# Kernel tuning notes

Measured on AMD Instinct MI355X. Metric: run time of the kernel, lower is better.

The kernel has to match this reference:

```python
import jax, jax.numpy as jnp
import numpy as np

D_IN, D_HID = 64, 128

def _ff(x, w1, b1, w2, b2):
    # FeedForward: Linear -> ReLU -> Linear
    return jax.nn.relu(x @ w1 + b1) @ w2 + b2

def setup_inputs() -> dict:
    key = jax.random.key(0)
    ks = jax.random.split(key, 10)
    N, m = 8, 2048
    def lin(k, fan_in, fan_out):
        bound = 1.0 / np.sqrt(fan_in)
        return jax.random.uniform(k, (fan_in, fan_out), jnp.float32, -bound, bound)
    return {
        "x": jax.random.normal(ks[0], (N, m, D_IN), jnp.float32),
        "edge": jax.random.uniform(ks[1], (N, m, m), jnp.float32),
        # f: dim_in -> dim_hid//2 -> dim_hid
        "f_w1": lin(ks[2], D_IN, D_HID // 2),
        "f_b1": jnp.zeros((D_HID // 2,), jnp.float32),
        "f_w2": lin(ks[3], D_HID // 2, D_HID),
        "f_b2": jnp.zeros((D_HID,), jnp.float32),
        # g: 2*dim_in -> dim_hid -> dim_hid
        "g_w1": lin(ks[4], 2 * D_IN, D_HID),
        "g_b1": jnp.zeros((D_HID,), jnp.float32),
        "g_w2": lin(ks[5], D_HID, D_HID),
        "g_b2": jnp.zeros((D_HID,), jnp.float32),
    }

def reference(x, edge, f_w1, f_b1, f_w2, f_b2, g_w1, g_b1, g_w2, g_b2):
    # self dynamics: f(x) -> [N, m, D_HID]
    self_dyn = _ff(x, f_w1, f_b1, f_w2, f_b2)
    # Original builds interaction[n,i,j] = cat(x[n,i], x[n,i]) (receiver is
    # transposed twice), so g is constant along j. Compute g once per sender node.
    gx = _ff(jnp.concatenate([x, x], axis=-1), g_w1, g_b1, g_w2, g_b2)  # [N, m, H]
    # interaction.sum over sender dim i with edge weights: out[n,j] = sum_i edge[n,i,j]*gx[n,i]
    inter = jnp.einsum('nij,nih->njh', edge, gx)
    return self_dyn + inter
```

## Files before the change

### kernel.cpp

```cpp
#include <hip/hip_runtime.h>


typedef __attribute__((ext_vector_type(8))) short bf16x8;
typedef __attribute__((ext_vector_type(8))) unsigned short u16x8;
typedef __attribute__((ext_vector_type(4))) unsigned short u16x4;
typedef __attribute__((ext_vector_type(4))) float f32x4;
typedef __attribute__((ext_vector_type(8))) float f32x8;

static __device__ __forceinline__ unsigned short f2bf(float f) {
  union { float f; unsigned int i; } c; c.f = f;
  return (unsigned short)((c.i + 0x7fffu + ((c.i >> 16) & 1u)) >> 16);
}

__global__ __launch_bounds__(256) void k_gx(
    const float* __restrict__ x,
    const float* __restrict__ gw1,
    const float* __restrict__ gb1,
    const float* __restrict__ gw2,
    const float* __restrict__ gb2,
    unsigned short* __restrict__ gxT)
{
  __shared__ short xs[64 * 64];
  __shared__ short w1T[128 * 64];
  __shared__ short w2T[128 * 128];
  __shared__ short h2s[64 * 128];

  const int t = threadIdx.x;
  const int R0 = blockIdx.x * 64;

  for (int idx = t; idx < 64 * 128; idx += 256) {
    int k = idx >> 7, n = idx & 127;
    float v = gw1[idx] + gw1[64 * 128 + idx];
    w1T[(n << 6) + (((k >> 3) ^ (n & 7)) << 3) + (k & 7)] = (short)f2bf(v);
  }
  for (int idx = t; idx < 128 * 128; idx += 256) {
    int k = idx >> 7, n = idx & 127;
    w2T[(n << 7) + (((k >> 3) ^ (n & 7)) << 3) + (k & 7)] = (short)f2bf(gw2[idx]);
  }
  for (int s = t; s < 64 * 16; s += 256) {
    int row = s >> 4, c4 = s & 15;
    f32x4 v = *(const f32x4*)(x + (size_t)(R0 + row) * 64 + c4 * 4);
    u16x4 pk;
#pragma unroll
    for (int r = 0; r < 4; ++r) pk[r] = f2bf(v[r]);
    *(u16x4*)(xs + (row << 6) + (((c4 >> 1) ^ (row & 7)) << 3) + ((c4 & 1) << 2)) = pk;
  }
  __syncthreads();

  const int w = t >> 6, l = t & 63;
  const int lr = l & 15, q = l >> 4;
  const int mrow = w * 16 + lr;

  bf16x8 a[2];
#pragma unroll
  for (int ks = 0; ks < 2; ++ks) {
    int c = ks * 4 + q;
    a[ks] = *(const bf16x8*)(xs + (mrow << 6) + ((c ^ (mrow & 7)) << 3));
  }

  f32x4 acc;
#pragma unroll
  for (int nf = 0; nf < 8; ++nf) {
    acc = (f32x4){0.f, 0.f, 0.f, 0.f};
#pragma unroll
    for (int ks = 0; ks < 2; ++ks) {
      int c = ks * 4 + q;
      int nr = nf * 16 + lr;
      bf16x8 b = *(const bf16x8*)(w1T + (nr << 6) + ((c ^ (nr & 7)) << 3));
      acc = __builtin_amdgcn_mfma_f32_16x16x32_bf16(a[ks], b, acc, 0, 0, 0);
    }
    float bias = gb1[nf * 16 + lr];
#pragma unroll
    for (int r = 0; r < 4; ++r) {
      float v = acc[r] + bias;
      v = v > 0.f ? v : 0.f;
      int row = w * 16 + q * 4 + r, n = nf * 16 + lr;
      h2s[(row << 7) + (((n >> 3) ^ (row & 7)) << 3) + (n & 7)] = (short)f2bf(v);
    }
  }
  __syncthreads();

  bf16x8 a2[4];
#pragma unroll
  for (int ks = 0; ks < 4; ++ks) {
    int c = ks * 4 + q;
    a2[ks] = *(const bf16x8*)(h2s + (mrow << 7) + ((c ^ (mrow & 7)) << 3));
  }
  const int batch = R0 >> 11;
  const int ib = R0 & 2047;
#pragma unroll
  for (int nf = 0; nf < 8; ++nf) {
    acc = (f32x4){0.f, 0.f, 0.f, 0.f};
#pragma unroll
    for (int ks = 0; ks < 4; ++ks) {
      int c = ks * 4 + q;
      int nr = nf * 16 + lr;
      bf16x8 b = *(const bf16x8*)(w2T + (nr << 7) + ((c ^ (nr & 7)) << 3));
      acc = __builtin_amdgcn_mfma_f32_16x16x32_bf16(a2[ks], b, acc, 0, 0, 0);
    }
    float bias = gb2[nf * 16 + lr];
    u16x4 pk;
#pragma unroll
    for (int r = 0; r < 4; ++r) pk[r] = f2bf(acc[r] + bias);
    *(u16x4*)(gxT + (size_t)(batch * 128 + nf * 16 + lr) * 2048 + ib + w * 16 + q * 4) = pk;
  }
}

__device__ __forceinline__ void load_tiles(const float* ep, const unsigned short* gp,
                                           f32x8& er, u16x8 gr[4])
{
  er = *(const f32x8*)ep;
#pragma unroll
  for (int qq = 0; qq < 4; ++qq)
    gr[qq] = *(const u16x8*)(gp + (size_t)qq * 32 * 2048);
}

__global__ __launch_bounds__(256) void k_main(
    const float* __restrict__ edge,
    const unsigned short* __restrict__ gxT,
    const float* __restrict__ x,
    const float* __restrict__ fw1,
    const float* __restrict__ fb1,
    const float* __restrict__ fw2,
    const float* __restrict__ fb2,
    float* __restrict__ out)
{
  __shared__ short eT[32 * 72];
  __shared__ short bT[128 * 64];
  __shared__ short xs[32 * 64];
  __shared__ short w1T[64 * 64];
  __shared__ short h1s[32 * 64];

  const int t = threadIdx.x;
  const int batch = blockIdx.x & 7;
  const int j0 = (blockIdx.x >> 3) * 32;

  const int w = t >> 6, l = t & 63;
  const int wm = w & 1, wn = w >> 1;
  const int lr = l & 15, q = l >> 4;

  const int e_ii = t >> 2;
  const int e_cj = t & 3;
  const int g_hh = t >> 3;
  const int g_ci = t & 7;

  const float* ep = edge + (size_t)batch * 2048 * 2048 + (size_t)e_ii * 2048 + j0 + e_cj * 8;
  const unsigned short* gp = gxT + (size_t)batch * 128 * 2048 + (size_t)g_hh * 2048 + g_ci * 8;

  f32x4 acc[4];
#pragma unroll
  for (int nf = 0; nf < 4; ++nf) acc[nf] = (f32x4){0.f, 0.f, 0.f, 0.f};

  f32x8 er;
  u16x8 gr[4];
  load_tiles(ep, gp, er, gr);

  for (int kk = 0; kk < 32; ++kk) {
    __syncthreads();
#pragma unroll
    for (int u = 0; u < 8; ++u)
      eT[(e_cj * 8 + u) * 72 + (((e_ii >> 3) ^ e_cj) << 3) + (e_ii & 7)] = (short)f2bf(er[u]);
#pragma unroll
    for (int qq = 0; qq < 4; ++qq) {
      int r = qq * 32 + g_hh;
      *(u16x8*)(bT + (r << 6) + ((g_ci ^ (r & 7)) << 3)) = gr[qq];
    }
    __syncthreads();
    if (kk < 31) {
      ep += 64 * 2048; gp += 64;
      load_tiles(ep, gp, er, gr);
    }

#pragma unroll
    for (int ks = 0; ks < 2; ++ks) {
      const int c = ks * 4 + q;
      const int jj = wm * 16 + lr;
      bf16x8 a = *(const bf16x8*)(eT + jj * 72 + ((c ^ (jj >> 3)) << 3));
      bf16x8 b[4];
#pragma unroll
      for (int nf = 0; nf < 4; ++nf) {
        int h = wn * 64 + nf * 16 + lr;
        b[nf] = *(const bf16x8*)(bT + (h << 6) + ((c ^ (h & 7)) << 3));
      }
#pragma unroll
      for (int nf = 0; nf < 4; ++nf)
        acc[nf] = __builtin_amdgcn_mfma_f32_16x16x32_bf16(a, b[nf], acc[nf], 0, 0, 0);
    }
  }

  __syncthreads();
  for (int idx = t; idx < 64 * 64; idx += 256) {
    int k = idx >> 6, n = idx & 63;
    w1T[(n << 6) + (((k >> 3) ^ (n & 7)) << 3) + (k & 7)] = (short)f2bf(fw1[idx]);
  }
  for (int idx = t; idx < 64 * 128; idx += 256) {
    int k = idx >> 7, n = idx & 127;
    bT[(n << 6) + (((k >> 3) ^ (n & 7)) << 3) + (k & 7)] = (short)f2bf(fw2[idx]);
  }
  for (int s = t; s < 32 * 16; s += 256) {
    int row = s >> 4, c4 = s & 15;
    f32x4 v = *(const f32x4*)(x + (size_t)(batch * 2048 + j0 + row) * 64 + c4 * 4);
    u16x4 pk;
#pragma unroll
    for (int r = 0; r < 4; ++r) pk[r] = f2bf(v[r]);
    *(u16x4*)(xs + (row << 6) + (((c4 >> 1) ^ (row & 7)) << 3) + ((c4 & 1) << 2)) = pk;
  }
  __syncthreads();

  const int mrow = wm * 16 + lr;
  if (wn == 0) {
    bf16x8 a1[2];
#pragma unroll
    for (int ks = 0; ks < 2; ++ks) {
      int c = ks * 4 + q;
      a1[ks] = *(const bf16x8*)(xs + (mrow << 6) + ((c ^ (mrow & 7)) << 3));
    }
#pragma unroll
    for (int nf = 0; nf < 4; ++nf) {
      f32x4 h = (f32x4){0.f, 0.f, 0.f, 0.f};
#pragma unroll
      for (int ks = 0; ks < 2; ++ks) {
        int c = ks * 4 + q;
        int nr = nf * 16 + lr;
        bf16x8 b = *(const bf16x8*)(w1T + (nr << 6) + ((c ^ (nr & 7)) << 3));
        h = __builtin_amdgcn_mfma_f32_16x16x32_bf16(a1[ks], b, h, 0, 0, 0);
      }
      float bias = fb1[nf * 16 + lr];
#pragma unroll
      for (int r = 0; r < 4; ++r) {
        float v = h[r] + bias;
        v = v > 0.f ? v : 0.f;
        int row = wm * 16 + q * 4 + r, n = nf * 16 + lr;
        h1s[(row << 6) + (((n >> 3) ^ (row & 7)) << 3) + (n & 7)] = (short)f2bf(v);
      }
    }
  }
  __syncthreads();

  bf16x8 a2[2];
#pragma unroll
  for (int ks = 0; ks < 2; ++ks) {
    int c = ks * 4 + q;
    a2[ks] = *(const bf16x8*)(h1s + (mrow << 6) + ((c ^ (mrow & 7)) << 3));
  }
#pragma unroll
  for (int nf = 0; nf < 4; ++nf) {
    int h = wn * 64 + nf * 16 + lr;
#pragma unroll
    for (int ks = 0; ks < 2; ++ks) {
      int c = ks * 4 + q;
      bf16x8 b = *(const bf16x8*)(bT + (h << 6) + ((c ^ (h & 7)) << 3));
      acc[nf] = __builtin_amdgcn_mfma_f32_16x16x32_bf16(a2[ks], b, acc[nf], 0, 0, 0);
    }
    float bias = fb2[h];
#pragma unroll
    for (int r = 0; r < 4; ++r) {
      size_t o = ((size_t)batch * 2048 + j0 + wm * 16 + q * 4 + r) * 128 + h;
      out[o] = acc[nf][r] + bias;
    }
  }
}

extern "C" void kernel_launch(void* const* d_in, const int* in_sizes, int n_in,
                              void* d_out, int out_size, void* d_ws, size_t ws_size,
                              hipStream_t stream) {
  const float* x    = (const float*)d_in[0];
  const float* edge = (const float*)d_in[1];
  const float* fw1  = (const float*)d_in[2];
  const float* fb1  = (const float*)d_in[3];
  const float* fw2  = (const float*)d_in[4];
  const float* fb2  = (const float*)d_in[5];
  const float* gw1  = (const float*)d_in[6];
  const float* gb1  = (const float*)d_in[7];
  const float* gw2  = (const float*)d_in[8];
  const float* gb2  = (const float*)d_in[9];
  float* out = (float*)d_out;

  unsigned short* gxT = (unsigned short*)d_ws;

  hipLaunchKernelGGL(k_gx, dim3(256), dim3(256), 0, stream, x, gw1, gb1, gw2, gb2, gxT);
  hipLaunchKernelGGL(k_main, dim3(512), dim3(256), 0, stream, edge, gxT, x,
                     fw1, fb1, fw2, fb2, out);
}
```

Baseline: 240.1 us.

## Double-buffer edge tile in LDS and load gx B-fragments directly to registers

The main loop now double-buffers the transposed edge tile in shared memory, so each iteration needs one barrier instead of two. The gx operand is no longer staged through shared memory: each lane loads its MFMA B fragments straight from global memory into registers, prefetched one step ahead. Edge loads use nontemporal hints. This cuts LDS traffic and barriers but raises register pressure and loads gx with less coalesced per-lane global reads.

```diff
diff --git a/kernel.cpp b/kernel.cpp
--- a/kernel.cpp
+++ b/kernel.cpp
@@ -2,10 +2,8 @@
 
 
 typedef __attribute__((ext_vector_type(8))) short bf16x8;
-typedef __attribute__((ext_vector_type(8))) unsigned short u16x8;
 typedef __attribute__((ext_vector_type(4))) unsigned short u16x4;
 typedef __attribute__((ext_vector_type(4))) float f32x4;
-typedef __attribute__((ext_vector_type(8))) float f32x8;
 
 static __device__ __forceinline__ unsigned short f2bf(float f) {
   union { float f; unsigned int i; } c; c.f = f;
@@ -106,15 +104,6 @@
   }
 }
 
-__device__ __forceinline__ void load_tiles(const float* ep, const unsigned short* gp,
-                                           f32x8& er, u16x8 gr[4])
-{
-  er = *(const f32x8*)ep;
-#pragma unroll
-  for (int qq = 0; qq < 4; ++qq)
-    gr[qq] = *(const u16x8*)(gp + (size_t)qq * 32 * 2048);
-}
-
 __global__ __launch_bounds__(256) void k_main(
     const float* __restrict__ edge,
     const unsigned short* __restrict__ gxT,
@@ -125,7 +114,7 @@
     const float* __restrict__ fb2,
     float* __restrict__ out)
 {
-  __shared__ short eT[32 * 72];
+  __shared__ short eT[2][32 * 72];
   __shared__ short bT[128 * 64];
   __shared__ short xs[32 * 64];
   __shared__ short w1T[64 * 64];
@@ -141,54 +130,74 @@
 
   const int e_ii = t >> 2;
   const int e_cj = t & 3;
-  const int g_hh = t >> 3;
-  const int g_ci = t & 7;
 
   const float* ep = edge + (size_t)batch * 2048 * 2048 + (size_t)e_ii * 2048 + j0 + e_cj * 8;
-  const unsigned short* gp = gxT + (size_t)batch * 128 * 2048 + (size_t)g_hh * 2048 + g_ci * 8;
+  const unsigned short* gp = gxT + ((size_t)batch * 128 + wn * 64 + lr) * 2048 + q * 8;
 
   f32x4 acc[4];
 #pragma unroll
   for (int nf = 0; nf < 4; ++nf) acc[nf] = (f32x4){0.f, 0.f, 0.f, 0.f};
 
-  f32x8 er;
-  u16x8 gr[4];
-  load_tiles(ep, gp, er, gr);
-
-  for (int kk = 0; kk < 32; ++kk) {
-    __syncthreads();
-#pragma unroll
-    for (int u = 0; u < 8; ++u)
-      eT[(e_cj * 8 + u) * 72 + (((e_ii >> 3) ^ e_cj) << 3) + (e_ii & 7)] = (short)f2bf(er[u]);
-#pragma unroll
-    for (int qq = 0; qq < 4; ++qq) {
-      int r = qq * 32 + g_hh;
-      *(u16x8*)(bT + (r << 6) + ((g_ci ^ (r & 7)) << 3)) = gr[qq];
-    }
-    __syncthreads();
-    if (kk < 31) {
-      ep += 64 * 2048; gp += 64;
-      load_tiles(ep, gp, er, gr);
-    }
-
+  auto lde = [&](int kk, f32x4 er[2]) {
+    const float* p = ep + (size_t)kk * 64 * 2048;
+    er[0] = __builtin_nontemporal_load((const f32x4*)p);
+    er[1] = __builtin_nontemporal_load((const f32x4*)(p + 4));
+  };
+  auto ldg = [&](int kk, bf16x8 gf[8]) {
+    const unsigned short* p = gp + kk * 64;
+#pragma unroll
+    for (int nf = 0; nf < 4; ++nf)
+#pragma unroll
+      for (int ks = 0; ks < 2; ++ks)
+        gf[nf * 2 + ks] = *(const bf16x8*)(p + nf * 16 * 2048 + ks * 32);
+  };
+  auto st_e = [&](int buf, const f32x4 er[2]) {
+#pragma unroll
+    for (int u = 0; u < 8; ++u) {
+      float v = (u < 4) ? er[0][u & 3] : er[1][u & 3];
+      eT[buf][(e_cj * 8 + u) * 72 + (((e_ii >> 3) ^ e_cj) << 3) + (e_ii & 7)] = (short)f2bf(v);
+    }
+  };
+  auto comp = [&](int buf, const bf16x8 gf[8]) {
 #pragma unroll
     for (int ks = 0; ks < 2; ++ks) {
       const int c = ks * 4 + q;
       const int jj = wm * 16 + lr;
-      bf16x8 a = *(const bf16x8*)(eT + jj * 72 + ((c ^ (jj >> 3)) << 3));
-      bf16x8 b[4];
-#pragma unroll
-      for (int nf = 0; nf < 4; ++nf) {
-        int h = wn * 64 + nf * 16 + lr;
-        b[nf] = *(const bf16x8*)(bT + (h << 6) + ((c ^ (h & 7)) << 3));
-      }
+      bf16x8 a = *(const bf16x8*)(&eT[buf][jj * 72 + ((c ^ (jj >> 3)) << 3)]);
 #pragma unroll
       for (int nf = 0; nf < 4; ++nf)
-        acc[nf] = __builtin_amdgcn_mfma_f32_16x16x32_bf16(a, b[nf], acc[nf], 0, 0, 0);
-    }
-  }
-
-  __syncthreads();
+        acc[nf] = __builtin_amdgcn_mfma_f32_16x16x32_bf16(a, gf[nf * 2 + ks], acc[nf], 0, 0, 0);
+    }
+  };
+
+  f32x4 erA[2], erB[2];
+  bf16x8 gfA[8], gfB[8];
+
+  lde(0, erA);
+  ldg(0, gfA);
+  lde(1, erB);
+  st_e(0, erA);
+  __syncthreads();
+
+#pragma unroll 1
+  for (int mm = 0; mm < 15; ++mm) {
+    ldg(2 * mm + 1, gfB);
+    lde(2 * mm + 2, erA);
+    comp(0, gfA);
+    st_e(1, erB);
+    __syncthreads();
+    ldg(2 * mm + 2, gfA);
+    lde(2 * mm + 3, erB);
+    comp(1, gfB);
+    st_e(0, erA);
+    __syncthreads();
+  }
+  ldg(31, gfB);
+  comp(0, gfA);
+  st_e(1, erB);
+  __syncthreads();
+  comp(1, gfB);
+
   for (int idx = t; idx < 64 * 64; idx += 256) {
     int k = idx >> 6, n = idx & 63;
     w1T[(n << 6) + (((k >> 3) ^ (n & 7)) << 3) + (k & 7)] = (short)f2bf(fw1[idx]);
```

Result: slower. 280.5 us (+16.8%).
